# Performance work log

Hardware: AMD Instinct MI355X
Metric: run time of the kernel (lower is better)

Reference implementation:

```python
import jax, jax.numpy as jnp
import numpy as np

N = 30000        # nodes
E = 480000       # edges (before self-loops)
F_IN = 512       # input feature dim
HID = 64         # per-head hidden dim
HEADS = 4
WIDTH = HID * HEADS  # 256, concat heads
LAYERS = 3
NCLS = 40
NEG_SLOPE = 0.2


def setup_inputs() -> dict:
    key = jax.random.key(0)
    ks = jax.random.split(key, 16)
    def p(k, shape, scale=0.1):
        return jax.random.normal(k, shape, dtype=jnp.float32) * scale
    return {
        "x": jax.random.normal(ks[0], (N, F_IN), dtype=jnp.float32),
        "edge_index": jax.random.randint(ks[1], (2, E), 0, N, dtype=jnp.int32),
        # layer 1: F_IN -> HEADS*HID (concat)
        "W1": p(ks[2], (F_IN, WIDTH)), "as1": p(ks[3], (HEADS, HID)), "ad1": p(ks[4], (HEADS, HID)), "b1": p(ks[5], (WIDTH,)),
        # layer 2: WIDTH -> WIDTH
        "W2": p(ks[6], (WIDTH, WIDTH)), "as2": p(ks[7], (HEADS, HID)), "ad2": p(ks[8], (HEADS, HID)), "b2": p(ks[9], (WIDTH,)),
        # layer 3: WIDTH -> WIDTH
        "W3": p(ks[10], (WIDTH, WIDTH)), "as3": p(ks[11], (HEADS, HID)), "ad3": p(ks[12], (HEADS, HID)), "b3": p(ks[13], (WIDTH,)),
        # JK='cat' output head: WIDTH*LAYERS -> NCLS
        "Wo": p(ks[14], (WIDTH * LAYERS, NCLS)), "bo": p(ks[15], (NCLS,)),
    }


def gat_layer(x, Wm, a_src, a_dst, b, src, dst):
    # PyG GATConv (concat=True, eval mode): h = xW reshaped [N,H,C];
    # e_ij = leaky_relu(a_src.h_j + a_dst.h_i) for edge j->i, softmax over dst groups.
    n = x.shape[0]
    H, C = a_src.shape
    h = (x @ Wm).reshape(n, H, C)                      # [N,H,C]
    es = jnp.sum(h * a_src, axis=-1)                   # [N,H]
    ed = jnp.sum(h * a_dst, axis=-1)                   # [N,H]
    e = jax.nn.leaky_relu(es[src] + ed[dst], NEG_SLOPE)  # [Etot,H]
    m = jax.ops.segment_max(e, dst, num_segments=n)    # stable softmax per dst node
    w = jnp.exp(e - m[dst])
    den = jax.ops.segment_sum(w, dst, num_segments=n)
    alpha = w / den[dst]                               # [Etot,H]
    out = jax.ops.segment_sum(h[src] * alpha[:, :, None], dst, num_segments=n)  # [N,H,C]
    return out.reshape(n, H * C) + b


def reference(x, edge_index, W1, as1, ad1, b1, W2, as2, ad2, b2, W3, as3, ad3, b3, Wo, bo):
    # add self-loops (PyG GATConv default)
    loops = jnp.arange(N, dtype=edge_index.dtype)
    src = jnp.concatenate([edge_index[0], loops])
    dst = jnp.concatenate([edge_index[1], loops])
    # dropout is identity in eval mode
    h1 = jax.nn.relu(gat_layer(x, W1, as1, ad1, b1, src, dst))
    h2 = jax.nn.relu(gat_layer(h1, W2, as2, ad2, b2, src, dst))
    h3 = jax.nn.relu(gat_layer(h2, W3, as3, ad3, b3, src, dst))
    h = jnp.concatenate([h1, h2, h3], axis=-1)         # JK 'cat': [N, WIDTH*LAYERS]
    return h @ Wo + bo                                 # [N, NCLS]
```

## Files before the change

kernel.cpp:

```cpp
#include <hip/hip_runtime.h>

#define N_NODES 30000
#define N_EDGES 480000
#define ETOT    510000
#define F_IN    512
#define WIDTH   256
#define NCLS    40
#define KCAT    768
#define NPAD    48

typedef __attribute__((ext_vector_type(8))) short short8;
typedef __attribute__((ext_vector_type(4))) float f32x4;

__device__ __forceinline__ unsigned short f2bf(float f){
  unsigned u = __float_as_uint(f);
  u += 0x7fffu + ((u >> 16) & 1u);
  return (unsigned short)(u >> 16);
}
__device__ __forceinline__ float b2f(unsigned short s){
  return __uint_as_float(((unsigned)s) << 16);
}

__global__ void transpose_w_kernel(const float* __restrict__ W, unsigned short* __restrict__ Wt,
                                   int K, int Nc){
  int k = blockIdx.x * blockDim.x + threadIdx.x;
  int n = blockIdx.y;
  if (k < K) Wt[(size_t)n * K + k] = f2bf(W[(size_t)k * Nc + n]);
}

__global__ void transpose_wo_kernel(const float* __restrict__ Wo, unsigned short* __restrict__ WoT){
  int i = blockIdx.x * blockDim.x + threadIdx.x;
  if (i < NPAD * KCAT){
    int c = i / KCAT, k = i - c * KCAT;
    WoT[i] = (c < NCLS) ? f2bf(Wo[(size_t)k * NCLS + c]) : (unsigned short)0;
  }
}

__global__ void zero_kernel(int* __restrict__ p, int n){
  int i = blockIdx.x * blockDim.x + threadIdx.x;
  if (i < n) p[i] = 0;
}

__global__ void hist_kernel(const int* __restrict__ ei, int* __restrict__ counts){
  int e = blockIdx.x * blockDim.x + threadIdx.x;
  if (e < ETOT){
    int d = (e < N_EDGES) ? ei[N_EDGES + e] : (e - N_EDGES);
    atomicAdd(&counts[d], 1);
  }
}

__global__ __launch_bounds__(1024) void scan_kernel(const int* __restrict__ counts,
                                                    int* __restrict__ offsets,
                                                    int* __restrict__ cursor, int n){
  __shared__ int wsum[16];
  int tid = threadIdx.x, lane = tid & 63, wid = tid >> 6;
  int running = 0;
  int nchunks = (n + 1023) >> 10;
  for (int ch = 0; ch < nchunks; ++ch){
    int i = (ch << 10) + tid;
    int v = (i < n) ? counts[i] : 0;
    int x = v;
    #pragma unroll
    for (int off = 1; off < 64; off <<= 1){
      int t = __shfl_up(x, off, 64);
      if (lane >= off) x += t;
    }
    if (lane == 63) wsum[wid] = x;
    __syncthreads();
    if (wid == 0){
      int s = (lane < 16) ? wsum[lane] : 0;
      #pragma unroll
      for (int off = 1; off < 16; off <<= 1){
        int t = __shfl_up(s, off, 64);
        if (lane >= off) s += t;
      }
      if (lane < 16) wsum[lane] = s;
    }
    __syncthreads();
    int waveprefix = (wid > 0) ? wsum[wid - 1] : 0;
    int excl = x - v + waveprefix + running;
    if (i < n){ offsets[i] = excl; cursor[i] = excl; }
    running += wsum[15];
    __syncthreads();
  }
  if (tid == 0) offsets[n] = running;
}

__global__ void scatter_kernel(const int* __restrict__ ei, int* __restrict__ cursor,
                               int* __restrict__ srcs){
  int e = blockIdx.x * blockDim.x + threadIdx.x;
  if (e < ETOT){
    int s, d;
    if (e < N_EDGES){ s = ei[e]; d = ei[N_EDGES + e]; }
    else { s = e - N_EDGES; d = s; }
    int pos = atomicAdd(&cursor[d], 1);
    srcs[pos] = s;
  }
}

#define BM 64
#define BK 32
#define LDA 40

template<bool AF32>
__global__ __launch_bounds__(256) void gemm_fused_kernel(const void* __restrict__ Araw,
                                                         const unsigned short* __restrict__ Bt,
                                                         const float* __restrict__ a_s,
                                                         const float* __restrict__ a_d,
                                                         float* __restrict__ es,
                                                         float* __restrict__ ed,
                                                         unsigned short* __restrict__ hb,
                                                         int M, int K){
  __shared__ unsigned short Als[BM * LDA];
  __shared__ unsigned short Bls[256 * LDA];
  int tid = threadIdx.x;
  int lane = tid & 63, wid = tid >> 6;
  int l15 = lane & 15, quad = lane >> 4;
  int m0 = blockIdx.x * BM;

  f32x4 acc[16];
  #pragma unroll
  for (int t = 0; t < 16; ++t) acc[t] = (f32x4){0.f, 0.f, 0.f, 0.f};

  for (int k0 = 0; k0 < K; k0 += BK){
    __syncthreads();
    {
      int row = tid >> 2, g = tid & 3;
      int grow = m0 + row; if (grow >= M) grow = M - 1;
      if (AF32){
        const float* Af = (const float*)Araw + (size_t)grow * K + k0 + 8 * g;
        float4 v0 = *(const float4*)(Af);
        float4 v1 = *(const float4*)(Af + 4);
        ushort4 p0 = {f2bf(v0.x), f2bf(v0.y), f2bf(v0.z), f2bf(v0.w)};
        ushort4 p1 = {f2bf(v1.x), f2bf(v1.y), f2bf(v1.z), f2bf(v1.w)};
        *(ushort4*)(&Als[row * LDA + 8 * g])     = p0;
        *(ushort4*)(&Als[row * LDA + 8 * g + 4]) = p1;
      } else {
        const unsigned short* Ab = (const unsigned short*)Araw;
        uint4 av = *(const uint4*)(Ab + (size_t)grow * K + k0 + 8 * g);
        *(uint4*)(&Als[row * LDA + 8 * g]) = av;
      }
      const unsigned short* src = Bt + (size_t)tid * K + k0;
      uint4 b0 = *(const uint4*)(src);
      uint4 b1 = *(const uint4*)(src + 8);
      uint4 b2 = *(const uint4*)(src + 16);
      uint4 b3 = *(const uint4*)(src + 24);
      unsigned short* dst = &Bls[tid * LDA];
      *(uint4*)(dst) = b0;
      *(uint4*)(dst + 8) = b1;
      *(uint4*)(dst + 16) = b2;
      *(uint4*)(dst + 24) = b3;
    }
    __syncthreads();
    short8 af = *(const short8*)(&Als[(16 * wid + l15) * LDA + quad * 8]);
    #pragma unroll
    for (int t = 0; t < 16; ++t){
      short8 bf = *(const short8*)(&Bls[(16 * t + l15) * LDA + quad * 8]);
      acc[t] = __builtin_amdgcn_mfma_f32_16x16x32_bf16(af, bf, acc[t], 0, 0, 0);
    }
  }

  int row0 = m0 + 16 * wid + quad * 4;

  #pragma unroll
  for (int t = 0; t < 16; ++t){
    int col = 16 * t + l15;
    #pragma unroll
    for (int r = 0; r < 4; ++r){
      int grow = row0 + r;
      if (grow < M) hb[(size_t)grow * WIDTH + col] = f2bf(acc[t][r]);
    }
  }

  float as_v[16], ad_v[16];
  #pragma unroll
  for (int t = 0; t < 16; ++t){
    int cc = 16 * (t & 3) + l15;
    as_v[t] = a_s[(t >> 2) * 64 + cc];
    ad_v[t] = a_d[(t >> 2) * 64 + cc];
  }
  #pragma unroll
  for (int h = 0; h < 4; ++h){
    #pragma unroll
    for (int r = 0; r < 4; ++r){
      float se = 0.f, sd = 0.f;
      #pragma unroll
      for (int tt = 0; tt < 4; ++tt){
        int t = 4 * h + tt;
        se += acc[t][r] * as_v[t];
        sd += acc[t][r] * ad_v[t];
      }
      #pragma unroll
      for (int off = 1; off < 16; off <<= 1){
        se += __shfl_xor(se, off, 64);
        sd += __shfl_xor(sd, off, 64);
      }
      int grow = row0 + r;
      if (l15 == 0 && grow < M){
        es[grow * 4 + h] = se;
        ed[grow * 4 + h] = sd;
      }
    }
  }
}

__global__ __launch_bounds__(256) void agg_kernel(const int* __restrict__ offsets,
                                                  const int* __restrict__ srcs,
                                                  const float* __restrict__ es,
                                                  const float* __restrict__ ed,
                                                  const unsigned short* __restrict__ hb,
                                                  const float* __restrict__ bias,
                                                  unsigned short* __restrict__ hout){
  __shared__ float eLds[8][64][4];
  __shared__ int   sLds[8][64];
  int wid = threadIdx.x >> 6;
  int lane = threadIdx.x & 63;
  int half = lane >> 5, l32 = lane & 31;
  int slot = wid * 2 + half;
  int n = blockIdx.x * 8 + slot;
  int base = offsets[n];
  int deg = offsets[n + 1] - base;
  float4 edv = *(const float4*)(ed + n * 4);

  float m0 = -1e30f, m1 = -1e30f, m2 = -1e30f, m3 = -1e30f;
  for (int i = l32; i < deg; i += 32){
    int s = srcs[base + i];
    float4 ev = *(const float4*)(es + s * 4);
    float e0 = ev.x + edv.x, e1 = ev.y + edv.y, e2 = ev.z + edv.z, e3 = ev.w + edv.w;
    e0 = e0 > 0.f ? e0 : 0.2f * e0;
    e1 = e1 > 0.f ? e1 : 0.2f * e1;
    e2 = e2 > 0.f ? e2 : 0.2f * e2;
    e3 = e3 > 0.f ? e3 : 0.2f * e3;
    if (i < 64){
      sLds[slot][i] = s;
      *(float4*)(&eLds[slot][i][0]) = (float4){e0, e1, e2, e3};
    }
    m0 = fmaxf(m0, e0); m1 = fmaxf(m1, e1); m2 = fmaxf(m2, e2); m3 = fmaxf(m3, e3);
  }
  #pragma unroll
  for (int off = 1; off < 32; off <<= 1){
    m0 = fmaxf(m0, __shfl_xor(m0, off, 64));
    m1 = fmaxf(m1, __shfl_xor(m1, off, 64));
    m2 = fmaxf(m2, __shfl_xor(m2, off, 64));
    m3 = fmaxf(m3, __shfl_xor(m3, off, 64));
  }
  int head = l32 >> 3;
  float mh  = (head == 0) ? m0 : (head == 1) ? m1 : (head == 2) ? m2 : m3;
  float edh = (head == 0) ? edv.x : (head == 1) ? edv.y : (head == 2) ? edv.z : edv.w;

  float2 a0 = {0.f,0.f}, a1 = {0.f,0.f}, a2 = {0.f,0.f}, a3 = {0.f,0.f};
  float den = 0.f;
  const unsigned short* hcol = hb + 8 * l32;
  for (int i = 0; i < deg; i += 8){
    int sidx[8]; float w[8];
    #pragma unroll
    for (int u = 0; u < 8; ++u){
      int idx = i + u;
      bool v = idx < deg;
      float le; int s;
      if (idx < 64 || !v){
        int ic = v ? idx : 0;
        if (ic >= 64) ic = 0;
        s  = sLds[slot][ic];
        le = eLds[slot][ic][head];
      } else {
        s = srcs[base + idx];
        float e = es[s * 4 + head] + edh;
        le = e > 0.f ? e : 0.2f * e;
      }
      sidx[u] = s;
      w[u] = v ? __expf(le - mh) : 0.f;
    }
    uint4 hv[8];
    #pragma unroll
    for (int u = 0; u < 8; ++u)
      hv[u] = *(const uint4*)(hcol + (size_t)sidx[u] * WIDTH);
    #pragma unroll
    for (int u = 0; u < 8; ++u){
      float wu = w[u];
      den += wu;
      a0.x += wu * __uint_as_float(hv[u].x << 16);
      a0.y += wu * __uint_as_float(hv[u].x & 0xffff0000u);
      a1.x += wu * __uint_as_float(hv[u].y << 16);
      a1.y += wu * __uint_as_float(hv[u].y & 0xffff0000u);
      a2.x += wu * __uint_as_float(hv[u].z << 16);
      a2.y += wu * __uint_as_float(hv[u].z & 0xffff0000u);
      a3.x += wu * __uint_as_float(hv[u].w << 16);
      a3.y += wu * __uint_as_float(hv[u].w & 0xffff0000u);
    }
  }
  float inv = 1.0f / den;
  const float* bp = bias + 8 * l32;
  float4 bv0 = *(const float4*)(bp);
  float4 bv1 = *(const float4*)(bp + 4);
  float o0 = fmaxf(a0.x * inv + bv0.x, 0.f);
  float o1 = fmaxf(a0.y * inv + bv0.y, 0.f);
  float o2 = fmaxf(a1.x * inv + bv0.z, 0.f);
  float o3 = fmaxf(a1.y * inv + bv0.w, 0.f);
  float o4 = fmaxf(a2.x * inv + bv1.x, 0.f);
  float o5 = fmaxf(a2.y * inv + bv1.y, 0.f);
  float o6 = fmaxf(a3.x * inv + bv1.z, 0.f);
  float o7 = fmaxf(a3.y * inv + bv1.w, 0.f);
  uint4 o;
  o.x = (unsigned)f2bf(o0) | ((unsigned)f2bf(o1) << 16);
  o.y = (unsigned)f2bf(o2) | ((unsigned)f2bf(o3) << 16);
  o.z = (unsigned)f2bf(o4) | ((unsigned)f2bf(o5) << 16);
  o.w = (unsigned)f2bf(o6) | ((unsigned)f2bf(o7) << 16);
  *(uint4*)(hout + (size_t)n * WIDTH + 8 * l32) = o;
}

__global__ __launch_bounds__(256) void out_gemm_kernel(const unsigned short* __restrict__ h1,
                                                       const unsigned short* __restrict__ h2,
                                                       const unsigned short* __restrict__ h3,
                                                       const unsigned short* __restrict__ WoT,
                                                       const float* __restrict__ bo,
                                                       float* __restrict__ out){
  int tid = threadIdx.x, lane = tid & 63, wid = tid >> 6;
  int l15 = lane & 15, quad = lane >> 4;
  int m0 = blockIdx.x * 64 + 16 * wid;

  f32x4 acc[3];
  #pragma unroll
  for (int t = 0; t < 3; ++t) acc[t] = (f32x4){0.f, 0.f, 0.f, 0.f};

  int arow = m0 + l15; if (arow >= N_NODES) arow = N_NODES - 1;

  #pragma unroll
  for (int part = 0; part < 3; ++part){
    const unsigned short* hp = (part == 0) ? h1 : (part == 1) ? h2 : h3;
    const unsigned short* ap = hp + (size_t)arow * WIDTH;
    #pragma unroll
    for (int k0 = 0; k0 < WIDTH; k0 += 32){
      short8 af = *(const short8*)(ap + k0 + quad * 8);
      int kk = part * WIDTH + k0;
      #pragma unroll
      for (int t = 0; t < 3; ++t){
        short8 bf = *(const short8*)(WoT + (size_t)(16 * t + l15) * KCAT + kk + quad * 8);
        acc[t] = __builtin_amdgcn_mfma_f32_16x16x32_bf16(af, bf, acc[t], 0, 0, 0);
      }
    }
  }

  int r0 = m0 + quad * 4;
  #pragma unroll
  for (int t = 0; t < 3; ++t){
    int col = 16 * t + l15;
    if (col < NCLS){
      float bc = bo[col];
      #pragma unroll
      for (int r = 0; r < 4; ++r){
        int grow = r0 + r;
        if (grow < N_NODES) out[(size_t)grow * NCLS + col] = acc[t][r] + bc;
      }
    }
  }
}

static inline size_t align256(size_t x){ return (x + 255) & ~(size_t)255; }

extern "C" void kernel_launch(void* const* d_in, const int* in_sizes, int n_in,
                              void* d_out, int out_size, void* d_ws, size_t ws_size,
                              hipStream_t stream) {
  const float* x   = (const float*)d_in[0];
  const int*   ei  = (const int*)  d_in[1];
  const float* W1  = (const float*)d_in[2];
  const float* as1 = (const float*)d_in[3];
  const float* ad1 = (const float*)d_in[4];
  const float* b1  = (const float*)d_in[5];
  const float* W2  = (const float*)d_in[6];
  const float* as2 = (const float*)d_in[7];
  const float* ad2 = (const float*)d_in[8];
  const float* b2  = (const float*)d_in[9];
  const float* W3  = (const float*)d_in[10];
  const float* as3 = (const float*)d_in[11];
  const float* ad3 = (const float*)d_in[12];
  const float* b3  = (const float*)d_in[13];
  const float* Wo  = (const float*)d_in[14];
  const float* bo  = (const float*)d_in[15];
  float* out = (float*)d_out;

  char* p = (char*)d_ws;
  auto take = [&](size_t bytes) -> char* { char* cur = p; p += align256(bytes); return cur; };

  unsigned short* Wt1   = (unsigned short*)take((size_t)WIDTH * F_IN * 2);
  unsigned short* Wt2   = (unsigned short*)take((size_t)WIDTH * WIDTH * 2);
  unsigned short* Wt3   = (unsigned short*)take((size_t)WIDTH * WIDTH * 2);
  unsigned short* WoT   = (unsigned short*)take((size_t)NPAD * KCAT * 2);
  unsigned short* hstage= (unsigned short*)take((size_t)N_NODES * WIDTH * 2);
  float*          es    = (float*)take((size_t)N_NODES * 4 * 4);
  float*          ed    = (float*)take((size_t)N_NODES * 4 * 4);
  unsigned short* h1b   = (unsigned short*)take((size_t)N_NODES * WIDTH * 2);
  unsigned short* h2b   = (unsigned short*)take((size_t)N_NODES * WIDTH * 2);
  unsigned short* h3b   = (unsigned short*)take((size_t)N_NODES * WIDTH * 2);
  int*            counts  = (int*)take((size_t)N_NODES * 4);
  int*            offsets = (int*)take((size_t)(N_NODES + 1) * 4);
  int*            cursor  = (int*)take((size_t)N_NODES * 4);
  int*            srcs    = (int*)take((size_t)ETOT * 4);

  transpose_w_kernel<<<dim3(F_IN / 256, WIDTH), 256, 0, stream>>>(W1, Wt1, F_IN, WIDTH);
  transpose_w_kernel<<<dim3(1, WIDTH), 256, 0, stream>>>(W2, Wt2, WIDTH, WIDTH);
  transpose_w_kernel<<<dim3(1, WIDTH), 256, 0, stream>>>(W3, Wt3, WIDTH, WIDTH);
  transpose_wo_kernel<<<(NPAD * KCAT + 255) / 256, 256, 0, stream>>>(Wo, WoT);

  zero_kernel<<<(N_NODES + 255) / 256, 256, 0, stream>>>(counts, N_NODES);
  hist_kernel<<<(ETOT + 255) / 256, 256, 0, stream>>>(ei, counts);
  scan_kernel<<<1, 1024, 0, stream>>>(counts, offsets, cursor, N_NODES);
  scatter_kernel<<<(ETOT + 255) / 256, 256, 0, stream>>>(ei, cursor, srcs);

  const int gemm_grid = (N_NODES + BM - 1) / BM;
  const int agg_grid  = N_NODES / 8;

  gemm_fused_kernel<true><<<gemm_grid, 256, 0, stream>>>(x, Wt1, as1, ad1, es, ed, hstage, N_NODES, F_IN);
  agg_kernel<<<agg_grid, 256, 0, stream>>>(offsets, srcs, es, ed, hstage, b1, h1b);
  gemm_fused_kernel<false><<<gemm_grid, 256, 0, stream>>>(h1b, Wt2, as2, ad2, es, ed, hstage, N_NODES, WIDTH);
  agg_kernel<<<agg_grid, 256, 0, stream>>>(offsets, srcs, es, ed, hstage, b2, h2b);
  gemm_fused_kernel<false><<<gemm_grid, 256, 0, stream>>>(h2b, Wt3, as3, ad3, es, ed, hstage, N_NODES, WIDTH);
  agg_kernel<<<agg_grid, 256, 0, stream>>>(offsets, srcs, es, ed, hstage, b3, h3b);

  out_gemm_kernel<<<gemm_grid, 256, 0, stream>>>(h1b, h2b, h3b, WoT, bo, out);
}
```

Before: 413.0 us.

## Restructure node GEMM into 16-row tiles with direct global operand loads

The fused GEMM now gives each block 16 rows and each wave 64 output columns, which is one attention head. Operands are read straight from global memory into MFMA registers, so the shared-memory staging and per-step barriers are gone, and K is a compile-time template parameter. Each wave computes the attention logits for its head without a cross-head reduction. Output goes through an LDS stage so the global stores are coalesced. The cost is that every block rereads the whole weight matrix from global/L2 with 16-byte strided loads, and there is less reuse per block (16 rows instead of 64).

Result: slower. 500.7 us (+21.2%).

```diff
diff --git a/kernel.cpp b/kernel.cpp
--- a/kernel.cpp
+++ b/kernel.cpp
@@ -98,109 +98,91 @@
   }
 }
 
-#define BM 64
-#define BK 32
-#define LDA 40
-
-template<bool AF32>
+#define SSTR 264
+
+template<int K, bool AF32>
 __global__ __launch_bounds__(256) void gemm_fused_kernel(const void* __restrict__ Araw,
                                                          const unsigned short* __restrict__ Bt,
                                                          const float* __restrict__ a_s,
                                                          const float* __restrict__ a_d,
                                                          float* __restrict__ es,
                                                          float* __restrict__ ed,
-                                                         unsigned short* __restrict__ hb,
-                                                         int M, int K){
-  __shared__ unsigned short Als[BM * LDA];
-  __shared__ unsigned short Bls[256 * LDA];
+                                                         unsigned short* __restrict__ hb){
+  __shared__ unsigned short stage[16 * SSTR];
   int tid = threadIdx.x;
-  int lane = tid & 63, wid = tid >> 6;
+  int lane = tid & 63, w = tid >> 6;
   int l15 = lane & 15, quad = lane >> 4;
-  int m0 = blockIdx.x * BM;
-
-  f32x4 acc[16];
-  #pragma unroll
-  for (int t = 0; t < 16; ++t) acc[t] = (f32x4){0.f, 0.f, 0.f, 0.f};
-
-  for (int k0 = 0; k0 < K; k0 += BK){
-    __syncthreads();
-    {
-      int row = tid >> 2, g = tid & 3;
-      int grow = m0 + row; if (grow >= M) grow = M - 1;
-      if (AF32){
-        const float* Af = (const float*)Araw + (size_t)grow * K + k0 + 8 * g;
-        float4 v0 = *(const float4*)(Af);
-        float4 v1 = *(const float4*)(Af + 4);
-        ushort4 p0 = {f2bf(v0.x), f2bf(v0.y), f2bf(v0.z), f2bf(v0.w)};
-        ushort4 p1 = {f2bf(v1.x), f2bf(v1.y), f2bf(v1.z), f2bf(v1.w)};
-        *(ushort4*)(&Als[row * LDA + 8 * g])     = p0;
-        *(ushort4*)(&Als[row * LDA + 8 * g + 4]) = p1;
-      } else {
-        const unsigned short* Ab = (const unsigned short*)Araw;
-        uint4 av = *(const uint4*)(Ab + (size_t)grow * K + k0 + 8 * g);
-        *(uint4*)(&Als[row * LDA + 8 * g]) = av;
-      }
-      const unsigned short* src = Bt + (size_t)tid * K + k0;
-      uint4 b0 = *(const uint4*)(src);
-      uint4 b1 = *(const uint4*)(src + 8);
-      uint4 b2 = *(const uint4*)(src + 16);
-      uint4 b3 = *(const uint4*)(src + 24);
-      unsigned short* dst = &Bls[tid * LDA];
-      *(uint4*)(dst) = b0;
-      *(uint4*)(dst + 8) = b1;
-      *(uint4*)(dst + 16) = b2;
-      *(uint4*)(dst + 24) = b3;
-    }
-    __syncthreads();
-    short8 af = *(const short8*)(&Als[(16 * wid + l15) * LDA + quad * 8]);
-    #pragma unroll
-    for (int t = 0; t < 16; ++t){
-      short8 bf = *(const short8*)(&Bls[(16 * t + l15) * LDA + quad * 8]);
-      acc[t] = __builtin_amdgcn_mfma_f32_16x16x32_bf16(af, bf, acc[t], 0, 0, 0);
-    }
-  }
-
-  int row0 = m0 + 16 * wid + quad * 4;
-
-  #pragma unroll
-  for (int t = 0; t < 16; ++t){
-    int col = 16 * t + l15;
-    #pragma unroll
-    for (int r = 0; r < 4; ++r){
-      int grow = row0 + r;
-      if (grow < M) hb[(size_t)grow * WIDTH + col] = f2bf(acc[t][r]);
-    }
-  }
-
-  float as_v[16], ad_v[16];
-  #pragma unroll
-  for (int t = 0; t < 16; ++t){
-    int cc = 16 * (t & 3) + l15;
-    as_v[t] = a_s[(t >> 2) * 64 + cc];
-    ad_v[t] = a_d[(t >> 2) * 64 + cc];
-  }
-  #pragma unroll
-  for (int h = 0; h < 4; ++h){
-    #pragma unroll
-    for (int r = 0; r < 4; ++r){
-      float se = 0.f, sd = 0.f;
-      #pragma unroll
-      for (int tt = 0; tt < 4; ++tt){
-        int t = 4 * h + tt;
-        se += acc[t][r] * as_v[t];
-        sd += acc[t][r] * ad_v[t];
-      }
-      #pragma unroll
-      for (int off = 1; off < 16; off <<= 1){
-        se += __shfl_xor(se, off, 64);
-        sd += __shfl_xor(sd, off, 64);
-      }
-      int grow = row0 + r;
-      if (l15 == 0 && grow < M){
-        es[grow * 4 + h] = se;
-        ed[grow * 4 + h] = sd;
-      }
-    }
+  int r0 = blockIdx.x * 16;
+  int c0 = w * 64;
+
+  const unsigned short* Bp0 = Bt + (size_t)(c0 + l15) * K + quad * 8;
+  const unsigned short* Bp1 = Bp0 + (size_t)16 * K;
+  const unsigned short* Bp2 = Bp0 + (size_t)32 * K;
+  const unsigned short* Bp3 = Bp0 + (size_t)48 * K;
+
+  const float* Af = (const float*)Araw + (size_t)(r0 + l15) * K + quad * 8;
+  const unsigned short* Ab = (const unsigned short*)Araw + (size_t)(r0 + l15) * K + quad * 8;
+
+  f32x4 acc0 = (f32x4){0.f,0.f,0.f,0.f};
+  f32x4 acc1 = acc0, acc2 = acc0, acc3 = acc0;
+
+  #pragma unroll 4
+  for (int k0 = 0; k0 < K; k0 += 32){
+    short8 a;
+    if constexpr (AF32){
+      float4 v0 = *(const float4*)(Af + k0);
+      float4 v1 = *(const float4*)(Af + k0 + 4);
+      a[0] = (short)f2bf(v0.x); a[1] = (short)f2bf(v0.y);
+      a[2] = (short)f2bf(v0.z); a[3] = (short)f2bf(v0.w);
+      a[4] = (short)f2bf(v1.x); a[5] = (short)f2bf(v1.y);
+      a[6] = (short)f2bf(v1.z); a[7] = (short)f2bf(v1.w);
+    } else {
+      a = *(const short8*)(Ab + k0);
+    }
+    short8 b0 = *(const short8*)(Bp0 + k0);
+    short8 b1 = *(const short8*)(Bp1 + k0);
+    short8 b2 = *(const short8*)(Bp2 + k0);
+    short8 b3 = *(const short8*)(Bp3 + k0);
+    acc0 = __builtin_amdgcn_mfma_f32_16x16x32_bf16(a, b0, acc0, 0, 0, 0);
+    acc1 = __builtin_amdgcn_mfma_f32_16x16x32_bf16(a, b1, acc1, 0, 0, 0);
+    acc2 = __builtin_amdgcn_mfma_f32_16x16x32_bf16(a, b2, acc2, 0, 0, 0);
+    acc3 = __builtin_amdgcn_mfma_f32_16x16x32_bf16(a, b3, acc3, 0, 0, 0);
+  }
+
+  int rbase = quad * 4;
+  float as0 = a_s[c0 + l15],      ad0 = a_d[c0 + l15];
+  float as1 = a_s[c0 + 16 + l15], ad1 = a_d[c0 + 16 + l15];
+  float as2 = a_s[c0 + 32 + l15], ad2 = a_d[c0 + 32 + l15];
+  float as3 = a_s[c0 + 48 + l15], ad3 = a_d[c0 + 48 + l15];
+
+  #pragma unroll
+  for (int r = 0; r < 4; ++r){
+    int srow = (rbase + r) * SSTR + c0 + l15;
+    stage[srow]      = f2bf(acc0[r]);
+    stage[srow + 16] = f2bf(acc1[r]);
+    stage[srow + 32] = f2bf(acc2[r]);
+    stage[srow + 48] = f2bf(acc3[r]);
+    float se = acc0[r]*as0 + acc1[r]*as1 + acc2[r]*as2 + acc3[r]*as3;
+    float sd = acc0[r]*ad0 + acc1[r]*ad1 + acc2[r]*ad2 + acc3[r]*ad3;
+    #pragma unroll
+    for (int off = 1; off < 16; off <<= 1){
+      se += __shfl_xor(se, off, 64);
+      sd += __shfl_xor(sd, off, 64);
+    }
+    if (l15 == 0){
+      int grow = r0 + rbase + r;
+      es[grow * 4 + w] = se;
+      ed[grow * 4 + w] = sd;
+    }
+  }
+
+  __syncthreads();
+  #pragma unroll
+  for (int p = 0; p < 2; ++p){
+    int i = (p * 256 + tid) * 8;
+    int row = i >> 8, col = i & 255;
+    uint4 v = *(const uint4*)(&stage[row * SSTR + col]);
+    *(uint4*)(hb + (size_t)(r0 + row) * WIDTH + col) = v;
   }
 }
 
@@ -407,15 +389,16 @@
   scan_kernel<<<1, 1024, 0, stream>>>(counts, offsets, cursor, N_NODES);
   scatter_kernel<<<(ETOT + 255) / 256, 256, 0, stream>>>(ei, cursor, srcs);
 
-  const int gemm_grid = (N_NODES + BM - 1) / BM;
+  const int gemm_grid = N_NODES / 16;
   const int agg_grid  = N_NODES / 8;
-
-  gemm_fused_kernel<true><<<gemm_grid, 256, 0, stream>>>(x, Wt1, as1, ad1, es, ed, hstage, N_NODES, F_IN);
+  const int out_grid  = (N_NODES + 63) / 64;
+
+  gemm_fused_kernel<F_IN, true><<<gemm_grid, 256, 0, stream>>>(x, Wt1, as1, ad1, es, ed, hstage);
   agg_kernel<<<agg_grid, 256, 0, stream>>>(offsets, srcs, es, ed, hstage, b1, h1b);
-  gemm_fused_kernel<false><<<gemm_grid, 256, 0, stream>>>(h1b, Wt2, as2, ad2, es, ed, hstage, N_NODES, WIDTH);
+  gemm_fused_kernel<WIDTH, false><<<gemm_grid, 256, 0, stream>>>(h1b, Wt2, as2, ad2, es, ed, hstage);
   agg_kernel<<<agg_grid, 256, 0, stream>>>(offsets, srcs, es, ed, hstage, b2, h2b);
-  gemm_fused_kernel<false><<<gemm_grid, 256, 0, stream>>>(h2b, Wt3, as3, ad3, es, ed, hstage, N_NODES, WIDTH);
+  gemm_fused_kernel<WIDTH, false><<<gemm_grid, 256, 0, stream>>>(h2b, Wt3, as3, ad3, es, ed, hstage);
   agg_kernel<<<agg_grid, 256, 0, stream>>>(offsets, srcs, es, ed, hstage, b3, h3b);
 
-  out_gemm_kernel<<<gemm_grid, 256, 0, stream>>>(h1b, h2b, h3b, WoT, bo, out);
-}
+  out_gemm_kernel<<<out_grid, 256, 0, stream>>>(h1b, h2b, h3b, WoT, bo, out);
+}
```

## Rewrite layer GEMMs as persistent kernels with register-resident weights and async A staging

Applied to the files above, without the earlier changes.

The per-layer GEMM becomes a persistent kernel. Each wave keeps its 32-column slice of the bf16 weight matrix in registers for the whole run, so B tiles are no longer reloaded through LDS for every row block. A tiles of 32 rows are double-buffered: global_load_lds DMA for the bf16 inputs, register prefetch with bf16 conversion for the fp32 input layer, both with an XOR swizzle in LDS. Outputs are staged in LDS for coalesced row stores, and es/ed are merged into one interleaved array so agg gets both from a single buffer. This raises register pressure considerably, especially with K=512 held in registers, and adds more complex sync.

After: 429.3 us. +3.9%, slower.

```diff
diff --git a/kernel.cpp b/kernel.cpp
--- a/kernel.cpp
+++ b/kernel.cpp
@@ -8,6 +8,7 @@
 #define NCLS    40
 #define KCAT    768
 #define NPAD    48
+#define TM      32
 
 typedef __attribute__((ext_vector_type(8))) short short8;
 typedef __attribute__((ext_vector_type(4))) float f32x4;
@@ -19,6 +20,12 @@
 }
 __device__ __forceinline__ float b2f(unsigned short s){
   return __uint_as_float(((unsigned)s) << 16);
+}
+
+__device__ __forceinline__ void gload_lds16(const void* g, void* l){
+  __builtin_amdgcn_global_load_lds(
+      (const __attribute__((address_space(1))) unsigned int*)g,
+      (__attribute__((address_space(3))) unsigned int*)l, 16, 0, 0);
 }
 
 __global__ void transpose_w_kernel(const float* __restrict__ W, unsigned short* __restrict__ Wt,
@@ -98,116 +105,179 @@
   }
 }
 
-#define BM 64
-#define BK 32
-#define LDA 40
-
-template<bool AF32>
-__global__ __launch_bounds__(256) void gemm_fused_kernel(const void* __restrict__ Araw,
-                                                         const unsigned short* __restrict__ Bt,
-                                                         const float* __restrict__ a_s,
-                                                         const float* __restrict__ a_d,
-                                                         float* __restrict__ es,
-                                                         float* __restrict__ ed,
-                                                         unsigned short* __restrict__ hb,
-                                                         int M, int K){
-  __shared__ unsigned short Als[BM * LDA];
-  __shared__ unsigned short Bls[256 * LDA];
+template<int K, bool AF32>
+__global__ __launch_bounds__(512, AF32 ? 2 : 4)
+void gemm_bres_kernel(const void* __restrict__ Araw,
+                      const unsigned short* __restrict__ Bt,
+                      const float* __restrict__ a_s,
+                      const float* __restrict__ a_d,
+                      float* __restrict__ esd,
+                      unsigned short* __restrict__ hb,
+                      int M, int ntiles){
+  constexpr int KT = K / 32;
+  constexpr int ROWB = K * 2;
+  constexpr int ABUF_US = AF32 ? (TM * K) : (2 * TM * K);
+  __shared__ unsigned short Abuf[ABUF_US];
+  __shared__ unsigned short hstage[TM * 256];
+  __shared__ float cmb[2][TM][8];
+
   int tid = threadIdx.x;
-  int lane = tid & 63, wid = tid >> 6;
+  int lane = tid & 63, w = tid >> 6;
   int l15 = lane & 15, quad = lane >> 4;
-  int m0 = blockIdx.x * BM;
-
-  f32x4 acc[16];
-  #pragma unroll
-  for (int t = 0; t < 16; ++t) acc[t] = (f32x4){0.f, 0.f, 0.f, 0.f};
-
-  for (int k0 = 0; k0 < K; k0 += BK){
+  int c0 = w * 32;
+
+  short8 Bf[KT][2];
+  #pragma unroll
+  for (int kt = 0; kt < KT; ++kt){
+    #pragma unroll
+    for (int ct = 0; ct < 2; ++ct){
+      Bf[kt][ct] = *(const short8*)(Bt + (size_t)(c0 + ct*16 + l15) * K + kt*32 + quad*8);
+    }
+  }
+  float as_v[2], ad_v[2];
+  #pragma unroll
+  for (int ct = 0; ct < 2; ++ct){
+    as_v[ct] = a_s[c0 + ct*16 + l15];
+    ad_v[ct] = a_d[c0 + ct*16 + l15];
+  }
+
+  int t = blockIdx.x;
+  if (t >= ntiles) return;
+  int stride = gridDim.x;
+
+  auto dma_stage = [&](int tt, int bufsel){
+    unsigned short* bufb = Abuf + bufsel * (TM * K);
+    const char* Ab = (const char*)Araw;
+    constexpr int NCH = (TM * K * 2) / (512 * 16);
+    #pragma unroll
+    for (int c = 0; c < NCH; ++c){
+      int L = (c * 512 + tid) * 16;
+      int row = L / ROWB;
+      int colb = L % ROWB;
+      int grow = tt * TM + row; if (grow > M - 1) grow = M - 1;
+      const char* src = Ab + (size_t)grow * ROWB + (colb ^ ((row & 7) << 4));
+      gload_lds16(src, (char*)bufb + L);
+    }
+  };
+
+  uint4 va[8];
+  auto issue_loads = [&](int tt){
+    const char* xb = (const char*)Araw;
+    #pragma unroll
+    for (int i = 0; i < 8; ++i){
+      int L32 = (i * 512 + tid) * 16;
+      int row = L32 >> 11;
+      int colb = L32 & 2047;
+      int grow = tt * TM + row; if (grow > M - 1) grow = M - 1;
+      va[i] = *(const uint4*)(xb + (size_t)grow * 2048 + colb);
+    }
+  };
+  auto commit_stage = [&](){
+    #pragma unroll
+    for (int i = 0; i < 8; ++i){
+      int ob = (i * 512 + tid) * 8;
+      int row = ob >> 10;
+      unsigned u0 = (unsigned)f2bf(__uint_as_float(va[i].x)) |
+                    ((unsigned)f2bf(__uint_as_float(va[i].y)) << 16);
+      unsigned u1 = (unsigned)f2bf(__uint_as_float(va[i].z)) |
+                    ((unsigned)f2bf(__uint_as_float(va[i].w)) << 16);
+      uint2 uv; uv.x = u0; uv.y = u1;
+      *(uint2*)((char*)Abuf + (ob ^ ((row & 7) << 4))) = uv;
+    }
+  };
+
+  int cur = 0;
+  if constexpr (AF32){
+    issue_loads(t);
+    commit_stage();
+  } else {
+    dma_stage(t, 0);
+  }
+  __syncthreads();
+
+  while (true){
+    int nxt = t + stride;
+    if constexpr (AF32){
+      if (nxt < ntiles) issue_loads(nxt);
+    } else {
+      if (nxt < ntiles) dma_stage(nxt, cur ^ 1);
+    }
+
+    const unsigned short* buf = Abuf + (AF32 ? 0 : cur * (TM * K));
+    f32x4 acc[2][2];
+    #pragma unroll
+    for (int s = 0; s < 2; ++s)
+      #pragma unroll
+      for (int ct = 0; ct < 2; ++ct)
+        acc[s][ct] = (f32x4){0.f, 0.f, 0.f, 0.f};
+
+    #pragma unroll
+    for (int s = 0; s < 2; ++s){
+      int row = s * 16 + l15;
+      int swzus = (row & 7) << 3;
+      #pragma unroll
+      for (int kt = 0; kt < KT; ++kt){
+        short8 af = *(const short8*)(buf + row * K + ((kt * 32 + quad * 8) ^ swzus));
+        acc[s][0] = __builtin_amdgcn_mfma_f32_16x16x32_bf16(af, Bf[kt][0], acc[s][0], 0, 0, 0);
+        acc[s][1] = __builtin_amdgcn_mfma_f32_16x16x32_bf16(af, Bf[kt][1], acc[s][1], 0, 0, 0);
+      }
+    }
+
+    #pragma unroll
+    for (int s = 0; s < 2; ++s){
+      #pragma unroll
+      for (int r = 0; r < 4; ++r){
+        int row = s * 16 + quad * 4 + r;
+        #pragma unroll
+        for (int ct = 0; ct < 2; ++ct){
+          int colb = (c0 + ct * 16 + l15) * 2;
+          *(unsigned short*)((char*)hstage + row * 512 + (colb ^ ((row & 7) << 4)))
+              = f2bf(acc[s][ct][r]);
+        }
+        float se = acc[s][0][r] * as_v[0] + acc[s][1][r] * as_v[1];
+        float sd = acc[s][0][r] * ad_v[0] + acc[s][1][r] * ad_v[1];
+        #pragma unroll
+        for (int off = 1; off < 16; off <<= 1){
+          se += __shfl_xor(se, off, 64);
+          sd += __shfl_xor(sd, off, 64);
+        }
+        if (l15 == 0){ cmb[0][row][w] = se; cmb[1][row][w] = sd; }
+      }
+    }
     __syncthreads();
-    {
-      int row = tid >> 2, g = tid & 3;
-      int grow = m0 + row; if (grow >= M) grow = M - 1;
-      if (AF32){
-        const float* Af = (const float*)Araw + (size_t)grow * K + k0 + 8 * g;
-        float4 v0 = *(const float4*)(Af);
-        float4 v1 = *(const float4*)(Af + 4);
-        ushort4 p0 = {f2bf(v0.x), f2bf(v0.y), f2bf(v0.z), f2bf(v0.w)};
-        ushort4 p1 = {f2bf(v1.x), f2bf(v1.y), f2bf(v1.z), f2bf(v1.w)};
-        *(ushort4*)(&Als[row * LDA + 8 * g])     = p0;
-        *(ushort4*)(&Als[row * LDA + 8 * g + 4]) = p1;
-      } else {
-        const unsigned short* Ab = (const unsigned short*)Araw;
-        uint4 av = *(const uint4*)(Ab + (size_t)grow * K + k0 + 8 * g);
-        *(uint4*)(&Als[row * LDA + 8 * g]) = av;
-      }
-      const unsigned short* src = Bt + (size_t)tid * K + k0;
-      uint4 b0 = *(const uint4*)(src);
-      uint4 b1 = *(const uint4*)(src + 8);
-      uint4 b2 = *(const uint4*)(src + 16);
-      uint4 b3 = *(const uint4*)(src + 24);
-      unsigned short* dst = &Bls[tid * LDA];
-      *(uint4*)(dst) = b0;
-      *(uint4*)(dst + 8) = b1;
-      *(uint4*)(dst + 16) = b2;
-      *(uint4*)(dst + 24) = b3;
+
+    int r0 = t * TM;
+    #pragma unroll
+    for (int c = 0; c < 2; ++c){
+      int us = (c * 512 + tid) * 8;
+      int row = us >> 8;
+      int colb = (us & 255) * 2;
+      if (r0 + row < M){
+        uint4 v = *(const uint4*)((const char*)hstage + row * 512 + (colb ^ ((row & 7) << 4)));
+        *(uint4*)(hb + (size_t)(r0 + row) * 256 + (colb >> 1)) = v;
+      }
+    }
+    if (tid < 256){
+      int row = tid >> 3, j = tid & 7, hd = j >> 1, sel = j & 1;
+      if (r0 + row < M){
+        float v = cmb[sel][row][2 * hd] + cmb[sel][row][2 * hd + 1];
+        esd[(size_t)(r0 + row) * 8 + sel * 4 + hd] = v;
+      }
+    }
+
+    if (nxt >= ntiles) break;
+    if constexpr (AF32){
+      commit_stage();
     }
     __syncthreads();
-    short8 af = *(const short8*)(&Als[(16 * wid + l15) * LDA + quad * 8]);
-    #pragma unroll
-    for (int t = 0; t < 16; ++t){
-      short8 bf = *(const short8*)(&Bls[(16 * t + l15) * LDA + quad * 8]);
-      acc[t] = __builtin_amdgcn_mfma_f32_16x16x32_bf16(af, bf, acc[t], 0, 0, 0);
-    }
-  }
-
-  int row0 = m0 + 16 * wid + quad * 4;
-
-  #pragma unroll
-  for (int t = 0; t < 16; ++t){
-    int col = 16 * t + l15;
-    #pragma unroll
-    for (int r = 0; r < 4; ++r){
-      int grow = row0 + r;
-      if (grow < M) hb[(size_t)grow * WIDTH + col] = f2bf(acc[t][r]);
-    }
-  }
-
-  float as_v[16], ad_v[16];
-  #pragma unroll
-  for (int t = 0; t < 16; ++t){
-    int cc = 16 * (t & 3) + l15;
-    as_v[t] = a_s[(t >> 2) * 64 + cc];
-    ad_v[t] = a_d[(t >> 2) * 64 + cc];
-  }
-  #pragma unroll
-  for (int h = 0; h < 4; ++h){
-    #pragma unroll
-    for (int r = 0; r < 4; ++r){
-      float se = 0.f, sd = 0.f;
-      #pragma unroll
-      for (int tt = 0; tt < 4; ++tt){
-        int t = 4 * h + tt;
-        se += acc[t][r] * as_v[t];
-        sd += acc[t][r] * ad_v[t];
-      }
-      #pragma unroll
-      for (int off = 1; off < 16; off <<= 1){
-        se += __shfl_xor(se, off, 64);
-        sd += __shfl_xor(sd, off, 64);
-      }
-      int grow = row0 + r;
-      if (l15 == 0 && grow < M){
-        es[grow * 4 + h] = se;
-        ed[grow * 4 + h] = sd;
-      }
-    }
+    if constexpr (!AF32) cur ^= 1;
+    t = nxt;
   }
 }
 
 __global__ __launch_bounds__(256) void agg_kernel(const int* __restrict__ offsets,
                                                   const int* __restrict__ srcs,
-                                                  const float* __restrict__ es,
-                                                  const float* __restrict__ ed,
+                                                  const float* __restrict__ esd,
                                                   const unsigned short* __restrict__ hb,
                                                   const float* __restrict__ bias,
                                                   unsigned short* __restrict__ hout){
@@ -220,12 +290,12 @@
   int n = blockIdx.x * 8 + slot;
   int base = offsets[n];
   int deg = offsets[n + 1] - base;
-  float4 edv = *(const float4*)(ed + n * 4);
+  float4 edv = *(const float4*)(esd + (size_t)n * 8 + 4);
 
   float m0 = -1e30f, m1 = -1e30f, m2 = -1e30f, m3 = -1e30f;
   for (int i = l32; i < deg; i += 32){
     int s = srcs[base + i];
-    float4 ev = *(const float4*)(es + s * 4);
+    float4 ev = *(const float4*)(esd + (size_t)s * 8);
     float e0 = ev.x + edv.x, e1 = ev.y + edv.y, e2 = ev.z + edv.z, e3 = ev.w + edv.w;
     e0 = e0 > 0.f ? e0 : 0.2f * e0;
     e1 = e1 > 0.f ? e1 : 0.2f * e1;
@@ -252,7 +322,7 @@
   float den = 0.f;
   const unsigned short* hcol = hb + 8 * l32;
   for (int i = 0; i < deg; i += 8){
-    int sidx[8]; float w[8];
+    int sidx[8]; float wgt[8];
     #pragma unroll
     for (int u = 0; u < 8; ++u){
       int idx = i + u;
@@ -265,11 +335,11 @@
         le = eLds[slot][ic][head];
       } else {
         s = srcs[base + idx];
-        float e = es[s * 4 + head] + edh;
+        float e = esd[(size_t)s * 8 + head] + edh;
         le = e > 0.f ? e : 0.2f * e;
       }
       sidx[u] = s;
-      w[u] = v ? __expf(le - mh) : 0.f;
+      wgt[u] = v ? __expf(le - mh) : 0.f;
     }
     uint4 hv[8];
     #pragma unroll
@@ -277,7 +347,7 @@
       hv[u] = *(const uint4*)(hcol + (size_t)sidx[u] * WIDTH);
     #pragma unroll
     for (int u = 0; u < 8; ++u){
-      float wu = w[u];
+      float wu = wgt[u];
       den += wu;
       a0.x += wu * __uint_as_float(hv[u].x << 16);
       a0.y += wu * __uint_as_float(hv[u].x & 0xffff0000u);
@@ -386,9 +456,8 @@
   unsigned short* Wt2   = (unsigned short*)take((size_t)WIDTH * WIDTH * 2);
   unsigned short* Wt3   = (unsigned short*)take((size_t)WIDTH * WIDTH * 2);
   unsigned short* WoT   = (unsigned short*)take((size_t)NPAD * KCAT * 2);
-  unsigned short* hstage= (unsigned short*)take((size_t)N_NODES * WIDTH * 2);
-  float*          es    = (float*)take((size_t)N_NODES * 4 * 4);
-  float*          ed    = (float*)take((size_t)N_NODES * 4 * 4);
+  unsigned short* hs    = (unsigned short*)take((size_t)N_NODES * WIDTH * 2);
+  float*          esd   = (float*)take((size_t)N_NODES * 8 * 4);
   unsigned short* h1b   = (unsigned short*)take((size_t)N_NODES * WIDTH * 2);
   unsigned short* h2b   = (unsigned short*)take((size_t)N_NODES * WIDTH * 2);
   unsigned short* h3b   = (unsigned short*)take((size_t)N_NODES * WIDTH * 2);
@@ -407,15 +476,16 @@
   scan_kernel<<<1, 1024, 0, stream>>>(counts, offsets, cursor, N_NODES);
   scatter_kernel<<<(ETOT + 255) / 256, 256, 0, stream>>>(ei, cursor, srcs);
 
-  const int gemm_grid = (N_NODES + BM - 1) / BM;
-  const int agg_grid  = N_NODES / 8;
-
-  gemm_fused_kernel<true><<<gemm_grid, 256, 0, stream>>>(x, Wt1, as1, ad1, es, ed, hstage, N_NODES, F_IN);
-  agg_kernel<<<agg_grid, 256, 0, stream>>>(offsets, srcs, es, ed, hstage, b1, h1b);
-  gemm_fused_kernel<false><<<gemm_grid, 256, 0, stream>>>(h1b, Wt2, as2, ad2, es, ed, hstage, N_NODES, WIDTH);
-  agg_kernel<<<agg_grid, 256, 0, stream>>>(offsets, srcs, es, ed, hstage, b2, h2b);
-  gemm_fused_kernel<false><<<gemm_grid, 256, 0, stream>>>(h2b, Wt3, as3, ad3, es, ed, hstage, N_NODES, WIDTH);
-  agg_kernel<<<agg_grid, 256, 0, stream>>>(offsets, srcs, es, ed, hstage, b3, h3b);
-
-  out_gemm_kernel<<<gemm_grid, 256, 0, stream>>>(h1b, h2b, h3b, WoT, bo, out);
-}
+  const int ntiles = (N_NODES + TM - 1) / TM;
+  const int agg_grid = N_NODES / 8;
+  const int out_grid = (N_NODES + 63) / 64;
+
+  gemm_bres_kernel<F_IN, true><<<256, 512, 0, stream>>>(x, Wt1, as1, ad1, esd, hs, N_NODES, ntiles);
+  agg_kernel<<<agg_grid, 256, 0, stream>>>(offsets, srcs, esd, hs, b1, h1b);
+  gemm_bres_kernel<WIDTH, false><<<512, 512, 0, stream>>>(h1b, Wt2, as2, ad2, esd, hs, N_NODES, ntiles);
+  agg_kernel<<<agg_grid, 256, 0, stream>>>(offsets, srcs, esd, hs, b2, h2b);
+  gemm_bres_kernel<WIDTH, false><<<512, 512, 0, stream>>>(h2b, Wt3, as3, ad3, esd, hs, N_NODES, ntiles);
+  agg_kernel<<<agg_grid, 256, 0, stream>>>(offsets, srcs, esd, hs, b3, h3b);
+
+  out_gemm_kernel<<<out_grid, 256, 0, stream>>>(h1b, h2b, h3b, WoT, bo, out);
+}
```
